# Performance work log

Hardware: AMD Instinct MI355X
Metric: run time of the kernel (lower is better)

## Reference

```python
import jax, jax.numpy as jnp
import numpy as np

N, E, D = 40000, 640000, 128  # n_nodes, n_edges, hidden_dim
EPS = 1e-5  # equinox RMSNorm default eps


def setup_inputs() -> dict:
    key = jax.random.key(0)
    k1, k2, k3, k4 = jax.random.split(key, 4)
    x = jax.random.normal(k1, (N, D), dtype=jnp.float32)
    e = jax.random.randint(k2, (E, 2), 0, N)  # [E,2] int, col0=src, col1=dst
    W = jax.random.normal(k3, (D, D), dtype=jnp.float32) / np.sqrt(D).astype(np.float32)
    b = jax.random.normal(k4, (D,), dtype=jnp.float32) * 0.01
    g = jnp.ones((D,), dtype=jnp.float32)   # RMSNorm weight
    rb = jnp.zeros((D,), dtype=jnp.float32)  # RMSNorm bias
    return {"x": x, "e": e, "W": W, "b": b, "g": g, "rb": rb}


def reference(x, e, W, b, g, rb):
    src, dst = e[:, 0], e[:, 1]
    # gather source nodes, per-edge linear + relu  -> [E, D]
    m = jax.nn.relu(x[src] @ W.T + b)
    n = x.shape[0]
    # degree (any column of segment_sum(ones_like(m)) is the scalar degree)
    deg = jax.ops.segment_sum(jnp.ones((e.shape[0],), x.dtype), dst, num_segments=n)
    # max-aggregate messages to destination nodes  -> [N, D]
    agg = jax.ops.segment_max(m, dst, num_segments=n)
    agg = jnp.where(deg[:, None] == 0, jnp.zeros((), x.dtype), agg)
    # residual + RMSNorm
    h = x + agg
    inv = jax.lax.rsqrt(jnp.mean(h * h, axis=-1, keepdims=True) + EPS)
    return h * inv * g + rb
```

## Files before the change

kernel.cpp:

```cpp
#include <hip/hip_runtime.h>
#include <hip/hip_bf16.h>

#define D 128
#define EPS 1e-5f

typedef __bf16 bf16x8 __attribute__((ext_vector_type(8)));
typedef float  f32x4  __attribute__((ext_vector_type(4)));

__global__ __launch_bounds__(256) void gemm_relu_hist_kernel(
    const float* __restrict__ x, const float* __restrict__ W,
    const float* __restrict__ b, __bf16* __restrict__ y,
    const int* __restrict__ e, int* __restrict__ counts,
    int n, int E)
{
    __shared__ __attribute__((aligned(16))) __bf16 Wl[128][136];
    __shared__ __attribute__((aligned(16))) __bf16 xl[64][136];

    const int tid = threadIdx.x;
    const int block_row = blockIdx.x * 64;

    for (int i = tid; i < 4096; i += 256) {
        int r = i >> 5, q = i & 31;
        float4 v = ((const float4*)W)[i];
        __bf16* p = &Wl[r][q * 4];
        p[0] = (__bf16)v.x; p[1] = (__bf16)v.y;
        p[2] = (__bf16)v.z; p[3] = (__bf16)v.w;
    }
    for (int i = tid; i < 2048; i += 256) {
        int r = i >> 5, q = i & 31;
        int gr = block_row + r;
        float4 v = make_float4(0.f, 0.f, 0.f, 0.f);
        if (gr < n) v = ((const float4*)x)[(size_t)gr * 32 + q];
        __bf16* p = &xl[r][q * 4];
        p[0] = (__bf16)v.x; p[1] = (__bf16)v.y;
        p[2] = (__bf16)v.z; p[3] = (__bf16)v.w;
    }
    __syncthreads();

    {
        int base = blockIdx.x * 256 + tid;
        int stride = gridDim.x * 256;
#pragma unroll
        for (int t = 0; t < 4; t++) {
            int i = base + t * stride;
            if (i < E) atomicAdd(&counts[e[2 * i + 1]], 1);
        }
    }

    const int w  = tid >> 6;
    const int l  = tid & 63;
    const int lr = l & 15;
    const int lk = l >> 4;

    bf16x8 a[4];
#pragma unroll
    for (int ks = 0; ks < 4; ks++)
        a[ks] = *(const bf16x8*)&xl[w * 16 + lr][ks * 32 + lk * 8];

#pragma unroll
    for (int ct = 0; ct < 8; ct++) {
        f32x4 acc = {0.f, 0.f, 0.f, 0.f};
#pragma unroll
        for (int ks = 0; ks < 4; ks++) {
            bf16x8 bf = *(const bf16x8*)&Wl[ct * 16 + lr][ks * 32 + lk * 8];
            acc = __builtin_amdgcn_mfma_f32_16x16x32_bf16(a[ks], bf, acc, 0, 0, 0);
        }
        int col = ct * 16 + lr;
        float bias = b[col];
#pragma unroll
        for (int reg = 0; reg < 4; reg++) {
            int gr = block_row + w * 16 + lk * 4 + reg;
            if (gr < n)
                y[(size_t)gr * D + col] = (__bf16)fmaxf(acc[reg] + bias, 0.f);
        }
    }
}

__global__ __launch_bounds__(256) void scan_partial_kernel(
    const int* __restrict__ counts, int* __restrict__ row_start,
    int* __restrict__ partials, int n)
{
    __shared__ int s[256];
    const int tid = threadIdx.x;
    const int i = blockIdx.x * 256 + tid;
    int v = (i < n) ? counts[i] : 0;
    s[tid] = v;
    __syncthreads();
    for (int off = 1; off < 256; off <<= 1) {
        int add = (tid >= off) ? s[tid - off] : 0;
        __syncthreads();
        s[tid] += add;
        __syncthreads();
    }
    if (i < n) row_start[i] = s[tid] - v;
    if (tid == 255) partials[blockIdx.x] = s[255];
}

__global__ __launch_bounds__(256) void scan_add_kernel(
    int* __restrict__ row_start, const int* __restrict__ partials,
    int* __restrict__ cursor, int n, int nb)
{
    __shared__ int s[256];
    const int tid = threadIdx.x;
    int v = (tid < nb) ? partials[tid] : 0;
    s[tid] = v;
    __syncthreads();
    for (int off = 1; off < 256; off <<= 1) {
        int add = (tid >= off) ? s[tid - off] : 0;
        __syncthreads();
        s[tid] += add;
        __syncthreads();
    }
    int off0 = (blockIdx.x == 0) ? 0 : s[blockIdx.x - 1];

    int i = blockIdx.x * 256 + tid;
    if (i < n) {
        int val = row_start[i] + off0;
        row_start[i] = val;
        cursor[i]    = val;
    }
}

__global__ __launch_bounds__(256) void place_kernel(
    const int* __restrict__ e, int* __restrict__ cursor,
    int* __restrict__ sorted_src, int E)
{
    int i = blockIdx.x * 256 + threadIdx.x;
    if (i < E) {
        int2 ed = ((const int2*)e)[i];
        int pos = atomicAdd(&cursor[ed.y], 1);
        sorted_src[pos] = ed.x;
    }
}

__global__ __launch_bounds__(256) void seg_max_finalize_kernel(
    const int* __restrict__ row_start, const int* __restrict__ counts,
    const int* __restrict__ sorted_src, const unsigned int* __restrict__ ybu,
    const float* __restrict__ x, const float* __restrict__ g,
    const float* __restrict__ rb, float* __restrict__ out, int n)
{
    int row  = blockIdx.x * 4 + (threadIdx.x >> 6);
    int lane = threadIdx.x & 63;
    if (row >= n) return;

    const int start = row_start[row];
    const int cnt   = counts[row];

    float mx = 0.f, my = 0.f;
    int k = 0;
    for (; k + 3 < cnt; k += 4) {
        int s0 = sorted_src[start + k];
        int s1 = sorted_src[start + k + 1];
        int s2 = sorted_src[start + k + 2];
        int s3 = sorted_src[start + k + 3];
        unsigned int u0 = ybu[(size_t)s0 * 64 + lane];
        unsigned int u1 = ybu[(size_t)s1 * 64 + lane];
        unsigned int u2 = ybu[(size_t)s2 * 64 + lane];
        unsigned int u3 = ybu[(size_t)s3 * 64 + lane];
        mx = fmaxf(mx, fmaxf(fmaxf(__uint_as_float(u0 << 16),
                                   __uint_as_float(u1 << 16)),
                             fmaxf(__uint_as_float(u2 << 16),
                                   __uint_as_float(u3 << 16))));
        my = fmaxf(my, fmaxf(fmaxf(__uint_as_float(u0 & 0xffff0000u),
                                   __uint_as_float(u1 & 0xffff0000u)),
                             fmaxf(__uint_as_float(u2 & 0xffff0000u),
                                   __uint_as_float(u3 & 0xffff0000u))));
    }
    for (; k < cnt; k++) {
        int s0 = sorted_src[start + k];
        unsigned int u0 = ybu[(size_t)s0 * 64 + lane];
        mx = fmaxf(mx, __uint_as_float(u0 << 16));
        my = fmaxf(my, __uint_as_float(u0 & 0xffff0000u));
    }

    float2 xv = ((const float2*)(x + (size_t)row * D))[lane];
    float hx = xv.x + mx;
    float hy = xv.y + my;

    float ss = hx * hx + hy * hy;
#pragma unroll
    for (int off = 1; off < 64; off <<= 1) ss += __shfl_xor(ss, off);

    float inv = rsqrtf(ss * (1.0f / (float)D) + EPS);

    float2 gv = ((const float2*)g)[lane];
    float2 rv = ((const float2*)rb)[lane];
    float2 o  = make_float2(hx * inv * gv.x + rv.x,
                            hy * inv * gv.y + rv.y);
    ((float2*)(out + (size_t)row * D))[lane] = o;
}

extern "C" void kernel_launch(void* const* d_in, const int* in_sizes, int n_in,
                              void* d_out, int out_size, void* d_ws, size_t ws_size,
                              hipStream_t stream)
{
    const float* x  = (const float*)d_in[0];
    const int*   e  = (const int*)  d_in[1];
    const float* W  = (const float*)d_in[2];
    const float* b  = (const float*)d_in[3];
    const float* g  = (const float*)d_in[4];
    const float* rb = (const float*)d_in[5];
    float* out = (float*)d_out;

    const int n = in_sizes[0] / D;
    const int E = in_sizes[1] / 2;

    char* ws = (char*)d_ws;
    __bf16* y        = (__bf16*)(ws);
    int*   counts    = (int*)  (ws + 10240000);
    int*   row_start = (int*)  (ws + 10400000);
    int*   cursor    = (int*)  (ws + 10560000);
    int*   sorted_src= (int*)  (ws + 10720000);
    int*   partials  = (int*)  (ws + 13280000);

    const int nb = (n + 255) / 256;
    const int gblocks = (n + 63) / 64;

    hipMemsetAsync(counts, 0, (size_t)n * sizeof(int), stream);

    gemm_relu_hist_kernel<<<gblocks, 256, 0, stream>>>(x, W, b, y, e, counts, n, E);

    scan_partial_kernel<<<nb, 256, 0, stream>>>(counts, row_start, partials, n);
    scan_add_kernel<<<nb, 256, 0, stream>>>(row_start, partials, cursor, n, nb);
    place_kernel<<<(E + 255) / 256, 256, 0, stream>>>(e, cursor, sorted_src, E);

    seg_max_finalize_kernel<<<(n + 3) / 4, 256, 0, stream>>>(
        row_start, counts, sorted_src, (const unsigned int*)y, x, g, rb, out, n);
}
```

Baseline: 192.1 us.

## Split W conversion and histogram into prep kernel; GEMM reads bf16 W from global

Adds a prep kernel that converts W to bf16 once into workspace and computes the destination-degree histogram with a grid-stride loop. The GEMM kernel no longer stages W and x through shared memory: each block drops its full fp32 W load and conversion, loads x rows straight into registers, and reads the bf16 W fragments from global/L2. This removes per-block redundant W traffic and LDS staging at the cost of an extra kernel launch and uncoalesced-ish global reads of W fragments per wave.

```diff
diff --git a/kernel.cpp b/kernel.cpp
--- a/kernel.cpp
+++ b/kernel.cpp
@@ -5,71 +5,70 @@
 #define EPS 1e-5f
 
 typedef __bf16 bf16x8 __attribute__((ext_vector_type(8)));
+typedef __bf16 bf16x4 __attribute__((ext_vector_type(4)));
 typedef float  f32x4  __attribute__((ext_vector_type(4)));
 
-__global__ __launch_bounds__(256) void gemm_relu_hist_kernel(
-    const float* __restrict__ x, const float* __restrict__ W,
-    const float* __restrict__ b, __bf16* __restrict__ y,
-    const int* __restrict__ e, int* __restrict__ counts,
-    int n, int E)
-{
-    __shared__ __attribute__((aligned(16))) __bf16 Wl[128][136];
-    __shared__ __attribute__((aligned(16))) __bf16 xl[64][136];
-
-    const int tid = threadIdx.x;
-    const int block_row = blockIdx.x * 64;
-
-    for (int i = tid; i < 4096; i += 256) {
-        int r = i >> 5, q = i & 31;
-        float4 v = ((const float4*)W)[i];
-        __bf16* p = &Wl[r][q * 4];
-        p[0] = (__bf16)v.x; p[1] = (__bf16)v.y;
-        p[2] = (__bf16)v.z; p[3] = (__bf16)v.w;
-    }
-    for (int i = tid; i < 2048; i += 256) {
-        int r = i >> 5, q = i & 31;
-        int gr = block_row + r;
-        float4 v = make_float4(0.f, 0.f, 0.f, 0.f);
-        if (gr < n) v = ((const float4*)x)[(size_t)gr * 32 + q];
-        __bf16* p = &xl[r][q * 4];
-        p[0] = (__bf16)v.x; p[1] = (__bf16)v.y;
-        p[2] = (__bf16)v.z; p[3] = (__bf16)v.w;
-    }
-    __syncthreads();
-
-    {
-        int base = blockIdx.x * 256 + tid;
-        int stride = gridDim.x * 256;
-#pragma unroll
-        for (int t = 0; t < 4; t++) {
-            int i = base + t * stride;
-            if (i < E) atomicAdd(&counts[e[2 * i + 1]], 1);
-        }
-    }
-
-    const int w  = tid >> 6;
-    const int l  = tid & 63;
-    const int lr = l & 15;
-    const int lk = l >> 4;
+__global__ __launch_bounds__(256) void prep_kernel(
+    const float* __restrict__ W, __bf16* __restrict__ Wb,
+    const int* __restrict__ e, int* __restrict__ counts, int E)
+{
+    const int tid = blockIdx.x * 256 + threadIdx.x;
+
+    if (tid < 4096) {
+        float4 v = ((const float4*)W)[tid];
+        bf16x4 h;
+        h[0] = (__bf16)v.x; h[1] = (__bf16)v.y;
+        h[2] = (__bf16)v.z; h[3] = (__bf16)v.w;
+        ((bf16x4*)Wb)[tid] = h;
+    }
+
+    const int stride = gridDim.x * 256;
+    for (int i = tid; i < E; i += stride)
+        atomicAdd(&counts[e[2 * i + 1]], 1);
+}
+
+__global__ __launch_bounds__(256) void gemm_kernel(
+    const float* __restrict__ x, const __bf16* __restrict__ Wb,
+    const float* __restrict__ b, __bf16* __restrict__ y, int n)
+{
+    const int tid  = threadIdx.x;
+    const int w    = tid >> 6;
+    const int l    = tid & 63;
+    const int lr   = l & 15;
+    const int lk   = l >> 4;
+    const int row0 = blockIdx.x * 64 + w * 16;
+
+    int ar = row0 + lr;
+    if (ar >= n) ar = n - 1;
+    const float* xr = x + (size_t)ar * D;
 
     bf16x8 a[4];
 #pragma unroll
-    for (int ks = 0; ks < 4; ks++)
-        a[ks] = *(const bf16x8*)&xl[w * 16 + lr][ks * 32 + lk * 8];
+    for (int ks = 0; ks < 4; ks++) {
+        float4 v0 = *(const float4*)(xr + ks * 32 + lk * 8);
+        float4 v1 = *(const float4*)(xr + ks * 32 + lk * 8 + 4);
+        bf16x8 t;
+        t[0] = (__bf16)v0.x; t[1] = (__bf16)v0.y;
+        t[2] = (__bf16)v0.z; t[3] = (__bf16)v0.w;
+        t[4] = (__bf16)v1.x; t[5] = (__bf16)v1.y;
+        t[6] = (__bf16)v1.z; t[7] = (__bf16)v1.w;
+        a[ks] = t;
+    }
 
 #pragma unroll
     for (int ct = 0; ct < 8; ct++) {
         f32x4 acc = {0.f, 0.f, 0.f, 0.f};
 #pragma unroll
         for (int ks = 0; ks < 4; ks++) {
-            bf16x8 bf = *(const bf16x8*)&Wl[ct * 16 + lr][ks * 32 + lk * 8];
+            bf16x8 bf = *(const bf16x8*)(Wb + (ct * 16 + lr) * D + ks * 32 + lk * 8);
             acc = __builtin_amdgcn_mfma_f32_16x16x32_bf16(a[ks], bf, acc, 0, 0, 0);
         }
-        int col = ct * 16 + lr;
-        float bias = b[col];
+        const int col  = ct * 16 + lr;
+        const float bias = b[col];
+        const int gr0  = row0 + lk * 4;
 #pragma unroll
         for (int reg = 0; reg < 4; reg++) {
-            int gr = block_row + w * 16 + lk * 4 + reg;
+            int gr = gr0 + reg;
             if (gr < n)
                 y[(size_t)gr * D + col] = (__bf16)fmaxf(acc[reg] + bias, 0.f);
         }
@@ -212,13 +211,15 @@
     int*   cursor    = (int*)  (ws + 10560000);
     int*   sorted_src= (int*)  (ws + 10720000);
     int*   partials  = (int*)  (ws + 13280000);
+    __bf16* Wb       = (__bf16*)(ws + 13281280);
 
     const int nb = (n + 255) / 256;
-    const int gblocks = (n + 63) / 64;
 
     hipMemsetAsync(counts, 0, (size_t)n * sizeof(int), stream);
 
-    gemm_relu_hist_kernel<<<gblocks, 256, 0, stream>>>(x, W, b, y, e, counts, n, E);
+    prep_kernel<<<640, 256, 0, stream>>>(W, Wb, e, counts, E);
+
+    gemm_kernel<<<(n + 63) / 64, 256, 0, stream>>>(x, Wb, b, y, n);
 
     scan_partial_kernel<<<nb, 256, 0, stream>>>(counts, row_start, partials, n);
     scan_add_kernel<<<nb, 256, 0, stream>>>(row_start, partials, cursor, n, nb);
```

New measurement: 197.5 us. 2.8% more time.
